# Kernel tuning notes

Hardware: AMD Instinct MI355X
Metric: run time of the kernel (lower is better)

## Reference

```python
import jax, jax.numpy as jnp
import numpy as np

B, N, C, H = 8, 4096, 768, 8


def setup_inputs() -> dict:
    key = jax.random.key(0)
    k1, k2, k3 = jax.random.split(key, 3)
    x = jax.random.normal(k1, (B, N, C), dtype=jnp.float32)
    W_qkv = jax.random.normal(k2, (C, 3 * C), dtype=jnp.float32) * 0.02
    W_proj = jax.random.normal(k3, (C, C), dtype=jnp.float32) * 0.02
    b_proj = jnp.zeros((C,), dtype=jnp.float32)
    temp = jnp.ones((H, 1, 1), dtype=jnp.float32)
    return {"x": x, "W_qkv": W_qkv, "W_proj": W_proj, "b_proj": b_proj, "temp": temp}


def reference(x, W_qkv, W_proj, b_proj, temp):
    b, n, c = x.shape
    h = temp.shape[0]
    d = c // h
    # qkv: [B,N,3C] -> [B,N,H,D,3]  (matches tf.reshape split order)
    qkv = (x @ W_qkv).reshape(b, n, h, d, 3)
    q, k, v = qkv[..., 0], qkv[..., 1], qkv[..., 2]
    # L2-normalize along the patch axis (axis=1), as tf.linalg.normalize
    q = q / jnp.linalg.norm(q, axis=1, keepdims=True)
    k = k / jnp.linalg.norm(k, axis=1, keepdims=True)
    # channel-wise (cross-covariance) attention: [B,H,D,D]
    attn = jnp.einsum('bnhd,bnhe->bhde', q, k) * temp
    attn = jax.nn.softmax(attn, axis=-1)
    # apply to v and fold heads back: [B,N,C]
    y = jnp.einsum('bhde,bnhe->bnhd', attn, v).reshape(b, n, c)
    return y @ W_proj + b_proj
```

## Files before the change

kernel.cpp:

```cpp
#include <hip/hip_runtime.h>

typedef __attribute__((ext_vector_type(8))) short short8;
typedef __attribute__((ext_vector_type(4))) float f32x4;

__device__ inline unsigned short f2b(float f) {
  unsigned int u = __builtin_bit_cast(unsigned int, f);
  u = (u + 0x7FFFu + ((u >> 16) & 1u)) >> 16;
  return (unsigned short)u;
}
__device__ inline float b2f(unsigned short s) {
  unsigned int u = ((unsigned int)s) << 16;
  return __builtin_bit_cast(float, u);
}

__device__ inline void async16(const void* g, void* l) {
  __builtin_amdgcn_global_load_lds((__attribute__((address_space(1))) void*)(g),
                                   (__attribute__((address_space(3))) void*)(l), 16, 0, 0);
}

__global__ void cvt_x(const float4* __restrict__ x, ushort4* __restrict__ xb, int n4) {
  int i = blockIdx.x * blockDim.x + threadIdx.x;
  int stride = gridDim.x * blockDim.x;
  for (; i < n4; i += stride) {
    float4 v = x[i];
    ushort4 o;
    o.x = f2b(v.x); o.y = f2b(v.y); o.z = f2b(v.z); o.w = f2b(v.w);
    xb[i] = o;
  }
}

__global__ __launch_bounds__(256) void t_wqkv(const float* __restrict__ W, unsigned short* __restrict__ Wt) {
  __shared__ float tile[32][33];
  int j0 = blockIdx.x * 32, c0 = blockIdx.y * 32;
  int tx = threadIdx.x & 31, ty = threadIdx.x >> 5;
#pragma unroll
  for (int r = 0; r < 32; r += 8)
    tile[ty + r][tx] = W[(size_t)(c0 + ty + r) * 2304 + j0 + tx];
  __syncthreads();
#pragma unroll
  for (int r = 0; r < 32; r += 8) {
    int j = j0 + ty + r;
    int h = j / 288, rem = j - h * 288;
    int d = rem / 3, s = rem - d * 3;
    int jj = s * 768 + h * 96 + d;
    Wt[(size_t)jj * 768 + c0 + tx] = f2b(tile[tx][ty + r]);
  }
}

__global__ __launch_bounds__(256) void t_wproj(const float* __restrict__ W, unsigned short* __restrict__ Wt) {
  __shared__ float tile[32][33];
  int j0 = blockIdx.x * 32, c0 = blockIdx.y * 32;
  int tx = threadIdx.x & 31, ty = threadIdx.x >> 5;
#pragma unroll
  for (int r = 0; r < 32; r += 8)
    tile[ty + r][tx] = W[(size_t)(c0 + ty + r) * 768 + j0 + tx];
  __syncthreads();
#pragma unroll
  for (int r = 0; r < 32; r += 8)
    Wt[(size_t)(j0 + ty + r) * 768 + c0 + tx] = f2b(tile[tx][ty + r]);
}

__global__ __launch_bounds__(512, 2) void gemm_qkv(
    const unsigned short* __restrict__ A, const unsigned short* __restrict__ Bt,
    unsigned short* __restrict__ Q, unsigned short* __restrict__ Kd, unsigned short* __restrict__ V) {
  extern __shared__ __align__(16) unsigned short smem[];
  const int tid = threadIdx.x;
  const int wave = tid >> 6, lane = tid & 63;
  const int mlane = lane & 15, quad = lane >> 4;
  const int m0 = blockIdx.x * 256, n0 = blockIdx.y * 256;
  const int ah = wave >> 2;
  const int wm = ah * 128;
  const int wn = (wave & 3) * 64;
  const int bh = wn >> 7;
  const int bl = wn & 64;

  f32x4 acc[8][4] = {};

  auto stage = [&](int kt, int c) {
    const int k0 = kt * 64;
#pragma unroll
    for (int h = 0; h < 4; ++h) {
      const unsigned short* src = (h < 2) ? A : Bt;
      const int rbase = ((h < 2) ? m0 : n0) + (h & 1) * 128;
      unsigned short* ldsbase = smem + c * 32768 + h * 8192;
#pragma unroll
      for (int i = 0; i < 2; ++i) {
        int ebase = i * 512 + (wave << 6);
        int e = ebase + lane;
        int row = e >> 3;
        int slot = (e & 7) ^ (row & 7);
        async16(src + (size_t)(rbase + row) * 768 + k0 + slot * 8, ldsbase + ebase * 8);
      }
    }
  };

  auto rdA = [&](const unsigned short* base, int mh, int kk, int f) -> short8 {
    int r = mh * 64 + f * 16 + mlane;
    return *(const short8*)&base[r * 64 + ((kk * 32 + quad * 8) ^ ((r & 7) << 3))];
  };
  auto rdB = [&](const unsigned short* base, int kk, int j) -> short8 {
    int r = bl + j * 16 + mlane;
    return *(const short8*)&base[r * 64 + ((kk * 32 + quad * 8) ^ ((r & 7) << 3))];
  };

  stage(0, 0);
  stage(1, 1);
  asm volatile("s_waitcnt vmcnt(8)" ::: "memory");
  __builtin_amdgcn_sched_barrier(0);
  __builtin_amdgcn_s_barrier();

#pragma unroll 1
  for (int t = 0; t < 12; ++t) {
    const int c = t & 1;
    const unsigned short* Abase = smem + c * 32768 + ah * 8192;
    const unsigned short* Bbase = smem + c * 32768 + 16384 + bh * 8192;
    short8 a0[4], a1[4], b0[4], b1[4];

#pragma unroll
    for (int j = 0; j < 4; ++j) b0[j] = rdB(Bbase, 0, j);
#pragma unroll
    for (int f = 0; f < 4; ++f) a0[f] = rdA(Abase, 0, 0, f);
    asm volatile("s_waitcnt lgkmcnt(0)" ::: "memory");
    __builtin_amdgcn_sched_barrier(0);
    __builtin_amdgcn_s_setprio(1);
#pragma unroll
    for (int f = 0; f < 4; ++f)
#pragma unroll
      for (int j = 0; j < 4; ++j)
        acc[f][j] = __builtin_amdgcn_mfma_f32_16x16x32_bf16(a0[f], b0[j], acc[f][j], 0, 0, 0);
    __builtin_amdgcn_s_setprio(0);
    __builtin_amdgcn_s_barrier();

#pragma unroll
    for (int f = 0; f < 4; ++f) a1[f] = rdA(Abase, 1, 0, f);
#pragma unroll
    for (int j = 0; j < 4; ++j) b1[j] = rdB(Bbase, 1, j);
    asm volatile("s_waitcnt lgkmcnt(0)" ::: "memory");
    __builtin_amdgcn_sched_barrier(0);
    __builtin_amdgcn_s_setprio(1);
#pragma unroll
    for (int f = 0; f < 4; ++f)
#pragma unroll
      for (int j = 0; j < 4; ++j)
        acc[4 + f][j] = __builtin_amdgcn_mfma_f32_16x16x32_bf16(a1[f], b0[j], acc[4 + f][j], 0, 0, 0);
    __builtin_amdgcn_s_setprio(0);
    __builtin_amdgcn_s_barrier();

#pragma unroll
    for (int f = 0; f < 4; ++f) a0[f] = rdA(Abase, 0, 1, f);
#pragma unroll
    for (int f = 0; f < 4; ++f) a1[f] = rdA(Abase, 1, 1, f);
    asm volatile("s_waitcnt lgkmcnt(0)" ::: "memory");
    __builtin_amdgcn_sched_barrier(0);
    __builtin_amdgcn_s_setprio(1);
#pragma unroll
    for (int f = 0; f < 4; ++f)
#pragma unroll
      for (int j = 0; j < 4; ++j)
        acc[f][j] = __builtin_amdgcn_mfma_f32_16x16x32_bf16(a0[f], b1[j], acc[f][j], 0, 0, 0);
    __builtin_amdgcn_s_setprio(0);
    __builtin_amdgcn_s_barrier();

    if (t < 10) stage(t + 2, c);
    __builtin_amdgcn_s_setprio(1);
#pragma unroll
    for (int f = 0; f < 4; ++f)
#pragma unroll
      for (int j = 0; j < 4; ++j)
        acc[4 + f][j] = __builtin_amdgcn_mfma_f32_16x16x32_bf16(a1[f], b1[j], acc[4 + f][j], 0, 0, 0);
    __builtin_amdgcn_s_setprio(0);
    if (t < 10) {
      asm volatile("s_waitcnt vmcnt(8)" ::: "memory");
      __builtin_amdgcn_sched_barrier(0);
      __builtin_amdgcn_s_barrier();
    } else if (t == 10) {
      asm volatile("s_waitcnt vmcnt(0)" ::: "memory");
      __builtin_amdgcn_sched_barrier(0);
      __builtin_amdgcn_s_barrier();
    }
  }

  const int bb = m0 >> 12;
  const int nbase = (m0 & 4095) + wm + quad * 4;
  unsigned short* dstp[4];
  size_t cb[4];
#pragma unroll
  for (int j = 0; j < 4; ++j) {
    int jj = n0 + wn + j * 16 + mlane;
    int s = (jj >= 1536) ? 2 : (jj >= 768) ? 1 : 0;
    int hd = jj - s * 768;
    int h = hd / 96;
    int d = hd - h * 96;
    dstp[j] = (s == 0) ? Q : (s == 1) ? Kd : V;
    cb[j] = ((size_t)(bb * 8 + h) * 4096) * 96 + d;
  }
#pragma unroll
  for (int mf = 0; mf < 8; ++mf) {
    int n = nbase + (mf >> 2) * 64 + (mf & 3) * 16;
#pragma unroll
    for (int r = 0; r < 4; ++r) {
#pragma unroll
      for (int j = 0; j < 4; ++j)
        dstp[j][cb[j] + (size_t)(n + r) * 96] = f2b(acc[mf][j][r]);
    }
  }
}

__global__ __launch_bounds__(256) void attn_partial(
    const unsigned short* __restrict__ Q, const unsigned short* __restrict__ Kd,
    float* __restrict__ Spart, float* __restrict__ sq, float* __restrict__ sk) {
  int chunk = blockIdx.x;
  int bh = blockIdx.y;
  __shared__ __align__(16) unsigned short QT[96 * 72];
  __shared__ __align__(16) unsigned short KT[96 * 72];
  int t = threadIdx.x;
  int wave = t >> 6, lane = t & 63, mlane = lane & 15, quad = lane >> 4;
  int wrow = (wave >> 1) * 48, wcol = (wave & 1) * 48;
  f32x4 acc[3][3] = {};
  const unsigned int* qp = (const unsigned int*)(Q + (size_t)bh * 4096 * 96);
  const unsigned int* kp = (const unsigned int*)(Kd + (size_t)bh * 4096 * 96);
  int c = t % 48, rg = t / 48;
  int nbeg = chunk * 256;
  float aq0 = 0.f, aq1 = 0.f, ak0 = 0.f, ak1 = 0.f;
  for (int n0 = nbeg; n0 < nbeg + 256; n0 += 64) {
    __syncthreads();
    if (rg < 5) {
      for (int n = rg; n < 64; n += 5) {
        unsigned int qv = qp[(size_t)(n0 + n) * 48 + c];
        unsigned int kv = kp[(size_t)(n0 + n) * 48 + c];
        QT[(2 * c) * 72 + n] = (unsigned short)(qv & 0xffff);
        QT[(2 * c + 1) * 72 + n] = (unsigned short)(qv >> 16);
        KT[(2 * c) * 72 + n] = (unsigned short)(kv & 0xffff);
        KT[(2 * c + 1) * 72 + n] = (unsigned short)(kv >> 16);
        float q0 = b2f((unsigned short)(qv & 0xffff)), q1 = b2f((unsigned short)(qv >> 16));
        float k0 = b2f((unsigned short)(kv & 0xffff)), k1 = b2f((unsigned short)(kv >> 16));
        aq0 += q0 * q0; aq1 += q1 * q1; ak0 += k0 * k0; ak1 += k1 * k1;
      }
    }
    __syncthreads();
#pragma unroll
    for (int kk = 0; kk < 64; kk += 32) {
      short8 a[3], bf[3];
#pragma unroll
      for (int f = 0; f < 3; ++f)
        a[f] = *(const short8*)&QT[(wrow + f * 16 + mlane) * 72 + kk + quad * 8];
#pragma unroll
      for (int f = 0; f < 3; ++f)
        bf[f] = *(const short8*)&KT[(wcol + f * 16 + mlane) * 72 + kk + quad * 8];
#pragma unroll
      for (int i = 0; i < 3; ++i)
#pragma unroll
        for (int j = 0; j < 3; ++j)
          acc[i][j] = __builtin_amdgcn_mfma_f32_16x16x32_bf16(a[i], bf[j], acc[i][j], 0, 0, 0);
    }
  }
  if (rg < 5) {
    atomicAdd(&sq[bh * 96 + 2 * c], aq0);
    atomicAdd(&sq[bh * 96 + 2 * c + 1], aq1);
    atomicAdd(&sk[bh * 96 + 2 * c], ak0);
    atomicAdd(&sk[bh * 96 + 2 * c + 1], ak1);
  }
  float* dst = Spart + ((size_t)bh * 16 + chunk) * 9216;
#pragma unroll
  for (int i = 0; i < 3; ++i)
#pragma unroll
    for (int j = 0; j < 3; ++j)
#pragma unroll
      for (int r = 0; r < 4; ++r)
        dst[(wrow + i * 16 + quad * 4 + r) * 96 + wcol + j * 16 + mlane] = acc[i][j][r];
}

__global__ __launch_bounds__(256) void attn_finalize(
    const float* __restrict__ Spart, const float* __restrict__ sq,
    const float* __restrict__ sk, const float* __restrict__ temp,
    unsigned short* __restrict__ P) {
  int bh = blockIdx.x, h = bh & 7;
  __shared__ float S[9216];
  __shared__ float rk[96], rq[96];
  int t = threadIdx.x;
  const float* base = Spart + (size_t)bh * 16 * 9216;
  if (t < 96) {
    rk[t] = rsqrtf(sk[bh * 96 + t]);
    rq[t] = rsqrtf(sq[bh * 96 + t]) * temp[h];
  }
  __syncthreads();
  for (int i = t; i < 9216; i += 256) {
    float s = 0.f;
#pragma unroll
    for (int c2 = 0; c2 < 16; ++c2) s += base[(size_t)c2 * 9216 + i];
    int d = i / 96, e = i - d * 96;
    S[i] = s * rq[d] * rk[e];
  }
  __syncthreads();
  if (t < 96) {
    int d = t;
    float mx = -1e30f;
    for (int e = 0; e < 96; ++e) mx = fmaxf(mx, S[d * 96 + e]);
    float sum = 0.f;
    for (int e = 0; e < 96; ++e) {
      float v = expf(S[d * 96 + e] - mx);
      S[d * 96 + e] = v;
      sum += v;
    }
    float inv = 1.0f / sum;
    for (int e = 0; e < 96; ++e)
      P[(size_t)bh * 9216 + d * 96 + e] = f2b(S[d * 96 + e] * inv);
  }
}

__global__ __launch_bounds__(256) void gemm_pv(
    const unsigned short* __restrict__ V, const unsigned short* __restrict__ P,
    unsigned short* __restrict__ y) {
  int bh = blockIdx.y;
  int b = bh >> 3, h = bh & 7;
  int m0 = blockIdx.x * 128;
  int t = threadIdx.x, wave = t >> 6, lane = t & 63, mlane = lane & 15, quad = lane >> 4;
  const unsigned short* Vb = V + (size_t)bh * 4096 * 96;
  const unsigned short* Pb = P + (size_t)bh * 9216;
  f32x4 acc[2][6] = {};
#pragma unroll
  for (int kk = 0; kk < 96; kk += 32) {
    short8 a[2], bfr[6];
#pragma unroll
    for (int i = 0; i < 2; ++i)
      a[i] = *(const short8*)&Vb[(size_t)(m0 + wave * 32 + i * 16 + mlane) * 96 + kk + quad * 8];
#pragma unroll
    for (int j = 0; j < 6; ++j)
      bfr[j] = *(const short8*)&Pb[(j * 16 + mlane) * 96 + kk + quad * 8];
#pragma unroll
    for (int i = 0; i < 2; ++i)
#pragma unroll
      for (int j = 0; j < 6; ++j)
        acc[i][j] = __builtin_amdgcn_mfma_f32_16x16x32_bf16(a[i], bfr[j], acc[i][j], 0, 0, 0);
  }
#pragma unroll
  for (int i = 0; i < 2; ++i) {
    int n = m0 + wave * 32 + i * 16 + quad * 4;
#pragma unroll
    for (int j = 0; j < 6; ++j) {
      int d = j * 16 + mlane;
#pragma unroll
      for (int r = 0; r < 4; ++r)
        y[((size_t)b * 4096 + n + r) * 768 + h * 96 + d] = f2b(acc[i][j][r]);
    }
  }
}

__global__ __launch_bounds__(256) void gemm_proj(
    const unsigned short* __restrict__ A, const unsigned short* __restrict__ Bt,
    const float* __restrict__ bias, float* __restrict__ out) {
  __shared__ __align__(16) unsigned short As[128 * 64];
  __shared__ __align__(16) unsigned short Bs[128 * 64];
  const int tid = threadIdx.x;
  const int wave = tid >> 6, lane = tid & 63;
  const int mlane = lane & 15, quad = lane >> 4;
  const int m0 = blockIdx.x * 128, n0 = blockIdx.y * 128;
  const int wm = (wave >> 1) * 64, wn = (wave & 1) * 64;
  f32x4 acc[4][4] = {};
  for (int k0 = 0; k0 < 768; k0 += 64) {
    __syncthreads();
#pragma unroll
    for (int t = 0; t < 4; ++t) {
      int ebase = t * 256 + (wave << 6);
      int e = ebase + lane;
      int row = e >> 3, c8 = e & 7;
      async16(A + (size_t)(m0 + row) * 768 + k0 + c8 * 8, As + ebase * 8);
      async16(Bt + (size_t)(n0 + row) * 768 + k0 + c8 * 8, Bs + ebase * 8);
    }
    __syncthreads();
#pragma unroll
    for (int kk = 0; kk < 64; kk += 32) {
      short8 a[4], b[4];
#pragma unroll
      for (int f = 0; f < 4; ++f)
        a[f] = *(const short8*)&As[(wm + f * 16 + mlane) * 64 + kk + quad * 8];
#pragma unroll
      for (int f = 0; f < 4; ++f)
        b[f] = *(const short8*)&Bs[(wn + f * 16 + mlane) * 64 + kk + quad * 8];
#pragma unroll
      for (int i = 0; i < 4; ++i)
#pragma unroll
        for (int j = 0; j < 4; ++j)
          acc[i][j] = __builtin_amdgcn_mfma_f32_16x16x32_bf16(a[i], b[j], acc[i][j], 0, 0, 0);
    }
  }
#pragma unroll
  for (int fn = 0; fn < 4; ++fn) {
    int col = n0 + wn + fn * 16 + mlane;
    float bv = bias[col];
#pragma unroll
    for (int fm = 0; fm < 4; ++fm) {
      int m = m0 + wm + fm * 16 + quad * 4;
#pragma unroll
      for (int r = 0; r < 4; ++r)
        out[(size_t)(m + r) * 768 + col] = acc[fm][fn][r] + bv;
    }
  }
}

extern "C" void kernel_launch(void* const* d_in, const int* in_sizes, int n_in,
                              void* d_out, int out_size, void* d_ws, size_t ws_size,
                              hipStream_t stream) {
  const float* x = (const float*)d_in[0];
  const float* Wqkv = (const float*)d_in[1];
  const float* Wproj = (const float*)d_in[2];
  const float* bias = (const float*)d_in[3];
  const float* temp = (const float*)d_in[4];
  float* out = (float*)d_out;

  char* ws = (char*)d_ws;
  size_t off = 0;
  auto alloc = [&](size_t bytes) -> void* {
    void* p = ws + off;
    off += (bytes + 255) & ~(size_t)255;
    return p;
  };
  unsigned short* xb = (unsigned short*)alloc(32768ull * 768 * 2);
  unsigned short* Wtq = (unsigned short*)alloc(2304ull * 768 * 2);
  unsigned short* Wtp = (unsigned short*)alloc(768ull * 768 * 2);
  unsigned short* Q = (unsigned short*)alloc(64ull * 4096 * 96 * 2);
  unsigned short* Kd = (unsigned short*)alloc(64ull * 4096 * 96 * 2);
  unsigned short* V = (unsigned short*)alloc(64ull * 4096 * 96 * 2);
  float* sq = (float*)alloc(64 * 96 * 4);
  float* sk = (float*)alloc(64 * 96 * 4);
  unsigned short* P = (unsigned short*)alloc(64ull * 9216 * 2);
  (void)off; (void)ws_size; (void)in_sizes; (void)n_in; (void)out_size;

  float* Spart = out;

  static bool attr_set = false;
  if (!attr_set) {
    hipFuncSetAttribute((const void*)gemm_qkv, hipFuncAttributeMaxDynamicSharedMemorySize, 131072);
    attr_set = true;
  }

  cvt_x<<<4096, 256, 0, stream>>>((const float4*)x, (ushort4*)xb, 32768 * 768 / 4);
  t_wqkv<<<dim3(72, 24), 256, 0, stream>>>(Wqkv, Wtq);
  t_wproj<<<dim3(24, 24), 256, 0, stream>>>(Wproj, Wtp);
  hipMemsetAsync(sq, 0, 64 * 96 * 4, stream);
  hipMemsetAsync(sk, 0, 64 * 96 * 4, stream);
  gemm_qkv<<<dim3(128, 9), 512, 131072, stream>>>(xb, Wtq, Q, Kd, V);
  attn_partial<<<dim3(16, 64), 256, 0, stream>>>(Q, Kd, Spart, sq, sk);
  attn_finalize<<<64, 256, 0, stream>>>(Spart, sq, sk, temp, P);
  gemm_pv<<<dim3(32, 64), 256, 0, stream>>>(V, P, xb );
  gemm_proj<<<dim3(256, 6), 256, 0, stream>>>(xb , Wtp, bias, out);
}
```

Before: 490.0 us.

## Fold attention matrix into projection weights and fuse PV with output GEMM

Instead of computing y = P·V per head and then y·W_proj, the code precomputes per-batch fused weights M = P^T-combined W_proj (768x768 per batch) in a small kernel. It then runs one pipelined GEMM V·M directly producing the output with bias. This removes the intermediate y write/read and a separate GEMM pass. The output GEMM uses 256x256 tiles, double-buffered async LDS loads, XOR swizzle and priority scheduling. The cost is an extra small per-batch GEMM and bf16 rounding of the fused weights.

```diff
diff --git a/kernel.cpp b/kernel.cpp
--- a/kernel.cpp
+++ b/kernel.cpp
@@ -273,7 +273,7 @@
 __global__ __launch_bounds__(256) void attn_finalize(
     const float* __restrict__ Spart, const float* __restrict__ sq,
     const float* __restrict__ sk, const float* __restrict__ temp,
-    unsigned short* __restrict__ P) {
+    unsigned short* __restrict__ Pt) {
   int bh = blockIdx.x, h = bh & 7;
   __shared__ float S[9216];
   __shared__ float rk[96], rq[96];
@@ -304,26 +304,25 @@
     }
     float inv = 1.0f / sum;
     for (int e = 0; e < 96; ++e)
-      P[(size_t)bh * 9216 + d * 96 + e] = f2b(S[d * 96 + e] * inv);
-  }
-}
-
-__global__ __launch_bounds__(256) void gemm_pv(
-    const unsigned short* __restrict__ V, const unsigned short* __restrict__ P,
-    unsigned short* __restrict__ y) {
+      Pt[(size_t)bh * 9216 + e * 96 + d] = f2b(S[d * 96 + e] * inv);
+  }
+}
+
+__global__ __launch_bounds__(256) void m_pre(
+    const unsigned short* __restrict__ Wtp, const unsigned short* __restrict__ Pt,
+    unsigned short* __restrict__ Mt) {
   int bh = blockIdx.y;
   int b = bh >> 3, h = bh & 7;
   int m0 = blockIdx.x * 128;
   int t = threadIdx.x, wave = t >> 6, lane = t & 63, mlane = lane & 15, quad = lane >> 4;
-  const unsigned short* Vb = V + (size_t)bh * 4096 * 96;
-  const unsigned short* Pb = P + (size_t)bh * 9216;
+  const unsigned short* Pb = Pt + (size_t)bh * 9216;
   f32x4 acc[2][6] = {};
 #pragma unroll
   for (int kk = 0; kk < 96; kk += 32) {
     short8 a[2], bfr[6];
 #pragma unroll
     for (int i = 0; i < 2; ++i)
-      a[i] = *(const short8*)&Vb[(size_t)(m0 + wave * 32 + i * 16 + mlane) * 96 + kk + quad * 8];
+      a[i] = *(const short8*)&Wtp[(size_t)(m0 + wave * 32 + i * 16 + mlane) * 768 + h * 96 + kk + quad * 8];
 #pragma unroll
     for (int j = 0; j < 6; ++j)
       bfr[j] = *(const short8*)&Pb[(j * 16 + mlane) * 96 + kk + quad * 8];
@@ -335,65 +334,155 @@
   }
 #pragma unroll
   for (int i = 0; i < 2; ++i) {
-    int n = m0 + wave * 32 + i * 16 + quad * 4;
+    int cp = m0 + wave * 32 + i * 16 + quad * 4;
 #pragma unroll
     for (int j = 0; j < 6; ++j) {
-      int d = j * 16 + mlane;
+      int e = j * 16 + mlane;
 #pragma unroll
       for (int r = 0; r < 4; ++r)
-        y[((size_t)b * 4096 + n + r) * 768 + h * 96 + d] = f2b(acc[i][j][r]);
-    }
-  }
-}
-
-__global__ __launch_bounds__(256) void gemm_proj(
-    const unsigned short* __restrict__ A, const unsigned short* __restrict__ Bt,
+        Mt[((size_t)b * 768 + cp + r) * 768 + h * 96 + e] = f2b(acc[i][j][r]);
+    }
+  }
+}
+
+__global__ __launch_bounds__(512, 2) void gemm_out(
+    const unsigned short* __restrict__ V, const unsigned short* __restrict__ Mt,
     const float* __restrict__ bias, float* __restrict__ out) {
-  __shared__ __align__(16) unsigned short As[128 * 64];
-  __shared__ __align__(16) unsigned short Bs[128 * 64];
+  extern __shared__ __align__(16) unsigned short smem[];
   const int tid = threadIdx.x;
   const int wave = tid >> 6, lane = tid & 63;
   const int mlane = lane & 15, quad = lane >> 4;
-  const int m0 = blockIdx.x * 128, n0 = blockIdx.y * 128;
-  const int wm = (wave >> 1) * 64, wn = (wave & 1) * 64;
-  f32x4 acc[4][4] = {};
-  for (int k0 = 0; k0 < 768; k0 += 64) {
-    __syncthreads();
-#pragma unroll
-    for (int t = 0; t < 4; ++t) {
-      int ebase = t * 256 + (wave << 6);
-      int e = ebase + lane;
-      int row = e >> 3, c8 = e & 7;
-      async16(A + (size_t)(m0 + row) * 768 + k0 + c8 * 8, As + ebase * 8);
-      async16(Bt + (size_t)(n0 + row) * 768 + k0 + c8 * 8, Bs + ebase * 8);
-    }
-    __syncthreads();
-#pragma unroll
-    for (int kk = 0; kk < 64; kk += 32) {
-      short8 a[4], b[4];
-#pragma unroll
-      for (int f = 0; f < 4; ++f)
-        a[f] = *(const short8*)&As[(wm + f * 16 + mlane) * 64 + kk + quad * 8];
-#pragma unroll
-      for (int f = 0; f < 4; ++f)
-        b[f] = *(const short8*)&Bs[(wn + f * 16 + mlane) * 64 + kk + quad * 8];
-#pragma unroll
-      for (int i = 0; i < 4; ++i)
-#pragma unroll
-        for (int j = 0; j < 4; ++j)
-          acc[i][j] = __builtin_amdgcn_mfma_f32_16x16x32_bf16(a[i], b[j], acc[i][j], 0, 0, 0);
-    }
-  }
-#pragma unroll
-  for (int fn = 0; fn < 4; ++fn) {
-    int col = n0 + wn + fn * 16 + mlane;
+  const int m0 = blockIdx.x * 256, n0 = blockIdx.y * 256;
+  const int bb = m0 >> 12;
+  const int nloc0 = m0 & 4095;
+  const int ah = wave >> 2;
+  const int wm = ah * 128;
+  const int wn = (wave & 3) * 64;
+  const int bhf = wn >> 7;
+  const int bl = wn & 64;
+
+  f32x4 acc[8][4] = {};
+
+  auto stage = [&](int kt, int c) {
+#pragma unroll
+    for (int h = 0; h < 4; ++h) {
+      unsigned short* ldsbase = smem + c * 32768 + h * 8192;
+#pragma unroll
+      for (int i = 0; i < 2; ++i) {
+        int ebase = i * 512 + (wave << 6);
+        int e = ebase + lane;
+        int row = e >> 3;
+        int slot = (e & 7) ^ (row & 7);
+        if (h < 2) {
+          int kc = kt * 8 + slot;
+          int hh = kc / 12;
+          int e0 = (kc - hh * 12) * 8;
+          int n = nloc0 + (h & 1) * 128 + row;
+          async16(V + ((size_t)(bb * 8 + hh) * 4096 + n) * 96 + e0, ldsbase + ebase * 8);
+        } else {
+          int col = n0 + (h & 1) * 128 + row;
+          async16(Mt + ((size_t)bb * 768 + col) * 768 + kt * 64 + slot * 8, ldsbase + ebase * 8);
+        }
+      }
+    }
+  };
+
+  auto rdA = [&](const unsigned short* base, int mh, int kk, int f) -> short8 {
+    int r = mh * 64 + f * 16 + mlane;
+    return *(const short8*)&base[r * 64 + ((kk * 32 + quad * 8) ^ ((r & 7) << 3))];
+  };
+  auto rdB = [&](const unsigned short* base, int kk, int j) -> short8 {
+    int r = bl + j * 16 + mlane;
+    return *(const short8*)&base[r * 64 + ((kk * 32 + quad * 8) ^ ((r & 7) << 3))];
+  };
+
+  stage(0, 0);
+  stage(1, 1);
+  asm volatile("s_waitcnt vmcnt(8)" ::: "memory");
+  __builtin_amdgcn_sched_barrier(0);
+  __builtin_amdgcn_s_barrier();
+
+#pragma unroll 1
+  for (int t = 0; t < 12; ++t) {
+    const int c = t & 1;
+    const unsigned short* Abase = smem + c * 32768 + ah * 8192;
+    const unsigned short* Bbase = smem + c * 32768 + 16384 + bhf * 8192;
+    short8 a0[4], a1[4], b0[4], b1[4];
+
+#pragma unroll
+    for (int j = 0; j < 4; ++j) b0[j] = rdB(Bbase, 0, j);
+#pragma unroll
+    for (int f = 0; f < 4; ++f) a0[f] = rdA(Abase, 0, 0, f);
+    asm volatile("s_waitcnt lgkmcnt(0)" ::: "memory");
+    __builtin_amdgcn_sched_barrier(0);
+    __builtin_amdgcn_s_setprio(1);
+#pragma unroll
+    for (int f = 0; f < 4; ++f)
+#pragma unroll
+      for (int j = 0; j < 4; ++j)
+        acc[f][j] = __builtin_amdgcn_mfma_f32_16x16x32_bf16(a0[f], b0[j], acc[f][j], 0, 0, 0);
+    __builtin_amdgcn_s_setprio(0);
+    __builtin_amdgcn_s_barrier();
+
+#pragma unroll
+    for (int f = 0; f < 4; ++f) a1[f] = rdA(Abase, 1, 0, f);
+#pragma unroll
+    for (int j = 0; j < 4; ++j) b1[j] = rdB(Bbase, 1, j);
+    asm volatile("s_waitcnt lgkmcnt(0)" ::: "memory");
+    __builtin_amdgcn_sched_barrier(0);
+    __builtin_amdgcn_s_setprio(1);
+#pragma unroll
+    for (int f = 0; f < 4; ++f)
+#pragma unroll
+      for (int j = 0; j < 4; ++j)
+        acc[4 + f][j] = __builtin_amdgcn_mfma_f32_16x16x32_bf16(a1[f], b0[j], acc[4 + f][j], 0, 0, 0);
+    __builtin_amdgcn_s_setprio(0);
+    __builtin_amdgcn_s_barrier();
+
+#pragma unroll
+    for (int f = 0; f < 4; ++f) a0[f] = rdA(Abase, 0, 1, f);
+#pragma unroll
+    for (int f = 0; f < 4; ++f) a1[f] = rdA(Abase, 1, 1, f);
+    asm volatile("s_waitcnt lgkmcnt(0)" ::: "memory");
+    __builtin_amdgcn_sched_barrier(0);
+    __builtin_amdgcn_s_setprio(1);
+#pragma unroll
+    for (int f = 0; f < 4; ++f)
+#pragma unroll
+      for (int j = 0; j < 4; ++j)
+        acc[f][j] = __builtin_amdgcn_mfma_f32_16x16x32_bf16(a0[f], b1[j], acc[f][j], 0, 0, 0);
+    __builtin_amdgcn_s_setprio(0);
+    __builtin_amdgcn_s_barrier();
+
+    if (t < 10) stage(t + 2, c);
+    __builtin_amdgcn_s_setprio(1);
+#pragma unroll
+    for (int f = 0; f < 4; ++f)
+#pragma unroll
+      for (int j = 0; j < 4; ++j)
+        acc[4 + f][j] = __builtin_amdgcn_mfma_f32_16x16x32_bf16(a1[f], b1[j], acc[4 + f][j], 0, 0, 0);
+    __builtin_amdgcn_s_setprio(0);
+    if (t < 10) {
+      asm volatile("s_waitcnt vmcnt(8)" ::: "memory");
+      __builtin_amdgcn_sched_barrier(0);
+      __builtin_amdgcn_s_barrier();
+    } else if (t == 10) {
+      asm volatile("s_waitcnt vmcnt(0)" ::: "memory");
+      __builtin_amdgcn_sched_barrier(0);
+      __builtin_amdgcn_s_barrier();
+    }
+  }
+
+#pragma unroll
+  for (int j = 0; j < 4; ++j) {
+    int col = n0 + wn + j * 16 + mlane;
     float bv = bias[col];
 #pragma unroll
-    for (int fm = 0; fm < 4; ++fm) {
-      int m = m0 + wm + fm * 16 + quad * 4;
+    for (int mf = 0; mf < 8; ++mf) {
+      int m = m0 + wm + (mf >> 2) * 64 + (mf & 3) * 16 + quad * 4;
 #pragma unroll
       for (int r = 0; r < 4; ++r)
-        out[(size_t)(m + r) * 768 + col] = acc[fm][fn][r] + bv;
+        out[(size_t)(m + r) * 768 + col] = acc[mf][j][r] + bv;
     }
   }
 }
@@ -423,14 +512,17 @@
   unsigned short* V = (unsigned short*)alloc(64ull * 4096 * 96 * 2);
   float* sq = (float*)alloc(64 * 96 * 4);
   float* sk = (float*)alloc(64 * 96 * 4);
-  unsigned short* P = (unsigned short*)alloc(64ull * 9216 * 2);
+  unsigned short* Pt = (unsigned short*)alloc(64ull * 9216 * 2);
   (void)off; (void)ws_size; (void)in_sizes; (void)n_in; (void)out_size;
+
+  unsigned short* Mt = xb;
 
   float* Spart = out;
 
   static bool attr_set = false;
   if (!attr_set) {
     hipFuncSetAttribute((const void*)gemm_qkv, hipFuncAttributeMaxDynamicSharedMemorySize, 131072);
+    hipFuncSetAttribute((const void*)gemm_out, hipFuncAttributeMaxDynamicSharedMemorySize, 131072);
     attr_set = true;
   }
 
@@ -441,7 +533,7 @@
   hipMemsetAsync(sk, 0, 64 * 96 * 4, stream);
   gemm_qkv<<<dim3(128, 9), 512, 131072, stream>>>(xb, Wtq, Q, Kd, V);
   attn_partial<<<dim3(16, 64), 256, 0, stream>>>(Q, Kd, Spart, sq, sk);
-  attn_finalize<<<64, 256, 0, stream>>>(Spart, sq, sk, temp, P);
-  gemm_pv<<<dim3(32, 64), 256, 0, stream>>>(V, P, xb );
-  gemm_proj<<<dim3(256, 6), 256, 0, stream>>>(xb , Wtp, bias, out);
-}
+  attn_finalize<<<64, 256, 0, stream>>>(Spart, sq, sk, temp, Pt);
+  m_pre<<<dim3(6, 64), 256, 0, stream>>>(Wtp, Pt, Mt);
+  gemm_out<<<dim3(128, 3), 512, 131072, stream>>>(V, Mt, bias, out);
+}
```

Result: faster. 473.1 us (-3.5%).
